# Kernel optimization log

Measured on AMD Instinct MI355X. Metric: run time of the kernel, lower is better.

## Reference

```python
import jax, jax.numpy as jnp
import numpy as np

N = 100000   # nodes
E = 3200000  # edges (avg degree 32)
G = 512      # graphs in batch
F_IN = 10
H = 30


def setup_inputs() -> dict:
    key = jax.random.key(0)
    ks = jax.random.split(key, 14)
    x = jax.random.normal(ks[0], (N, F_IN), dtype=jnp.float32)
    edge_index = jax.random.randint(ks[1], (2, E), 0, N, dtype=jnp.int64)
    batch = jnp.sort(jax.random.randint(ks[2], (N,), 0, G, dtype=jnp.int64))
    edge_weights = jnp.ones((E,), dtype=jnp.float32)
    s = 0.1
    W1 = jax.random.normal(ks[3], (F_IN, H), jnp.float32) * s
    b1 = jnp.zeros((H,), jnp.float32)
    W2 = jax.random.normal(ks[4], (H, H), jnp.float32) * s
    b2 = jnp.zeros((H,), jnp.float32)
    W3 = jax.random.normal(ks[5], (H, H), jnp.float32) * s
    b3 = jnp.zeros((H,), jnp.float32)
    LW1 = jax.random.normal(ks[6], (H, 10), jnp.float32) * s
    Lb1 = jnp.zeros((10,), jnp.float32)
    LW2 = jax.random.normal(ks[7], (10, 2), jnp.float32) * s
    Lb2 = jnp.zeros((2,), jnp.float32)
    return dict(x=x, edge_index=edge_index, batch=batch, edge_weights=edge_weights,
                W1=W1, b1=b1, W2=W2, b2=b2, W3=W3, b3=b3,
                LW1=LW1, Lb1=Lb1, LW2=LW2, Lb2=Lb2)


def reference(x, edge_index, batch, edge_weights, W1, b1, W2, b2, W3, b3, LW1, Lb1, LW2, Lb2):
    n = x.shape[0]
    row, col = edge_index[0], edge_index[1]
    # PyG gcn_norm: add self-loops with weight 1, symmetric normalization
    loop = jnp.arange(n)
    row_f = jnp.concatenate([row, loop])
    col_f = jnp.concatenate([col, loop])
    w_f = jnp.concatenate([edge_weights, jnp.ones((n,), edge_weights.dtype)])
    deg = jax.ops.segment_sum(w_f, col_f, num_segments=n)
    dis = jnp.where(deg > 0, jax.lax.rsqrt(jnp.where(deg > 0, deg, 1.0)), 0.0)
    norm = dis[row_f] * w_f * dis[col_f]  # [E+N]

    def gcn(h, W, b):
        h = h @ W  # [N, out]
        agg = jax.ops.segment_sum(norm[:, None] * h[row_f], col_f, num_segments=n)
        return agg + b

    h = jax.nn.relu(gcn(x, W1, b1))
    h = jax.nn.relu(gcn(h, W2, b2))
    h = jax.nn.relu(gcn(h, W3, b3))  # embedding [N, 30]
    pooled = jax.ops.segment_max(h, batch, num_segments=G)  # [G, 30]
    out = jax.nn.relu(pooled @ LW1 + Lb1) @ LW2 + Lb2  # [G, 2]
    return out
```

## Files before the change

### kernel.cpp

```cpp
#include <hip/hip_runtime.h>
#include <hip/hip_bf16.h>
#include <hip/hip_fp16.h>


#define WG 256
#define CAP 9216
#define T_EDGES 16384

__global__ void k_init(int* bcur, float* pooled, int nb16, int pooledN) {
    int i = blockIdx.x * blockDim.x + threadIdx.x;
    if (i < nb16) bcur[i] = 0;
    if (i < pooledN) pooled[i] = 0.0f;
}

__global__ __launch_bounds__(1024)
void k_bucket(const int* __restrict__ row, const int* __restrict__ col,
              const float* __restrict__ w,
              int* bcur, int2* __restrict__ buck, int E, int NB) {
    __shared__ int hist[512];
    __shared__ int base[512];
    int tid = threadIdx.x;
    for (int i = tid; i < NB; i += 1024) hist[i] = 0;
    __syncthreads();
    int start = blockIdx.x * T_EDGES;
    int end = min(start + T_EDGES, E);
    for (int i = start + tid; i < end; i += 1024)
        atomicAdd(&hist[col[i] >> 8], 1);
    __syncthreads();
    for (int i = tid; i < NB; i += 1024) {
        int h = hist[i];
        base[i] = (h > 0) ? atomicAdd(&bcur[i * 16], h) : 0;
        hist[i] = 0;
    }
    __syncthreads();
    for (int i = start + tid; i < end; i += 1024) {
        int c = col[i];
        int b = c >> 8;
        int off = atomicAdd(&hist[b], 1);
        int pos = base[b] + off;
        if (pos < CAP) {
            int2 pk;
            pk.x = (c & 255) | (row[i] << 8);
            pk.y = __float_as_int(w[i]);
            buck[(size_t)b * CAP + pos] = pk;
        }
    }
}

__global__ __launch_bounds__(1024)
void k_fuse(const int* __restrict__ bcur, const int2* __restrict__ buck,
            float* __restrict__ dis, int* __restrict__ ptr,
            int2* __restrict__ csr, int N, int NB) {
    __shared__ int lc[256];
    __shared__ float lw[256];
    __shared__ int sh[256];
    __shared__ int cur[256];
    __shared__ int sb[512];
    int b = blockIdx.x;
    int tid = threadIdx.x;
    if (tid < 512) sb[tid] = (tid < NB) ? min(bcur[tid * 16], CAP) : 0;
    if (tid < 256) { lc[tid] = 0; lw[tid] = 0.0f; }
    __syncthreads();
    for (int off = 1; off < 512; off <<= 1) {
        int v = (tid < 512 && tid >= off) ? sb[tid - off] : 0;
        __syncthreads();
        if (tid < 512) sb[tid] += v;
        __syncthreads();
    }
    int m = min(bcur[b * 16], CAP);
    int bbase = sb[b] - m;
    if (b == 0 && tid == 0) ptr[N] = sb[511];
    const int2* bp = buck + (size_t)b * CAP;
    for (int i = tid; i < m; i += 1024) {
        int2 pk = bp[i];
        int lcol = pk.x & 255;
        atomicAdd(&lc[lcol], 1);
        atomicAdd(&lw[lcol], __int_as_float(pk.y));
    }
    __syncthreads();
    int lcnt = 0;
    if (tid < 256) { lcnt = lc[tid]; sh[tid] = lcnt; }
    __syncthreads();
    for (int off = 1; off < 256; off <<= 1) {
        int t = (tid >= off && tid < 256) ? sh[tid - off] : 0;
        __syncthreads();
        if (tid < 256) sh[tid] += t;
        __syncthreads();
    }
    int node = (b << 8) + tid;
    if (tid < 256) {
        int base = bbase + sh[tid] - lcnt;
        cur[tid] = base;
        if (node < N) {
            ptr[node] = base;
            float d = 1.0f + lw[tid];
            dis[node] = (d > 0.0f) ? (1.0f / sqrtf(d)) : 0.0f;
        }
    }
    __syncthreads();
    for (int i = tid; i < m; i += 1024) {
        int2 pk = bp[i];
        int lcol = pk.x & 255;
        int pos = atomicAdd(&cur[lcol], 1);
        int2 rec;
        rec.x = (int)(((unsigned)pk.x) >> 8);
        rec.y = pk.y;
        csr[pos] = rec;
    }
}

__global__ void k_stage(const float* __restrict__ x, const float* __restrict__ dis,
                        __half* __restrict__ xp, int n) {
    int gid = blockIdx.x * blockDim.x + threadIdx.x;
    int node = gid >> 4, f = gid & 15;
    if (node < n)
        xp[(size_t)node * 16 + f] = __float2half((f < 10) ? dis[node] * x[(size_t)node * 10 + f] : 0.0f);
}

__global__ __launch_bounds__(256, 4)
void k_agg16(const __half* __restrict__ xp, const float* __restrict__ dis,
             const int* __restrict__ ptr, const int2* __restrict__ csr,
             float* __restrict__ y, int n) {
    int wid = (blockIdx.x * blockDim.x + threadIdx.x) >> 6;
    int lane = threadIdx.x & 63;
    int f = lane & 15;
    int laneq = lane & 48;
    int node = 4 * wid + (lane >> 4);
    bool valid = node < n;
    int s = 0, e = 0;
    if (valid) { s = ptr[node]; e = ptr[node + 1]; }
    int len = e - s;
    int m01 = max(__shfl(len, 0, 64), __shfl(len, 16, 64));
    int m23 = max(__shfl(len, 32, 64), __shfl(len, 48, 64));
    int maxlen = max(m01, m23);
    float a0 = 0.0f, a1 = 0.0f, a2 = 0.0f, a3 = 0.0f;
    for (int off = 0; off < maxlen; off += 16) {
        int idxv = 0; float nrmv = 0.0f;
        if (off + f < len) {
            int2 v = csr[s + off + f];
            idxv = v.x;
            nrmv = __int_as_float(v.y);
        }
        float wt[16], vt[16];
#pragma unroll
        for (int j = 0; j < 16; j++) {
            int r = __shfl(idxv, laneq | j, 64);
            wt[j] = __shfl(nrmv, laneq | j, 64);
            vt[j] = __half2float(xp[(size_t)r * 16 + f]);
        }
#pragma unroll
        for (int j = 0; j < 16; j += 4) {
            a0 = fmaf(wt[j],     vt[j],     a0);
            a1 = fmaf(wt[j + 1], vt[j + 1], a1);
            a2 = fmaf(wt[j + 2], vt[j + 2], a2);
            a3 = fmaf(wt[j + 3], vt[j + 3], a3);
        }
    }
    if (valid) {
        float acc = (a0 + a1) + (a2 + a3);
        float r = dis[node] * (acc + __half2float(xp[(size_t)node * 16 + f]));
        y[(size_t)node * 16 + f] = r;
    }
}

__global__ __launch_bounds__(256)
void k_lin1(const float* __restrict__ y, const float* __restrict__ W1,
            const float* __restrict__ b1, const float* __restrict__ W2,
            const float* __restrict__ dis, __half* __restrict__ out, int n) {
    __shared__ float W1s[10 * 32];
    __shared__ float W2s[30 * 32];
    __shared__ float b1s[32];
    __shared__ float ys[8][16];
    __shared__ float hs[8][32];
    int tid = threadIdx.x;
    for (int i = tid; i < 10 * 32; i += 256) { int k = i >> 5, f = i & 31; W1s[i] = (f < 30) ? W1[k * 30 + f] : 0.0f; }
    for (int i = tid; i < 30 * 32; i += 256) { int k = i >> 5, f = i & 31; W2s[i] = (f < 30) ? W2[k * 30 + f] : 0.0f; }
    if (tid < 32) b1s[tid] = (tid < 30) ? b1[tid] : 0.0f;
    int n8 = tid >> 5, f = tid & 31;
    int node = blockIdx.x * 8 + n8;
    __syncthreads();
    if (node < n && f < 16) ys[n8][f] = y[(size_t)node * 16 + f];
    __syncthreads();
    if (node < n) {
        float h = b1s[f];
#pragma unroll
        for (int k = 0; k < 10; k++) h += ys[n8][k] * W1s[k * 32 + f];
        h = fmaxf(h, 0.0f);
        if (f >= 30) h = 0.0f;
        hs[n8][f] = h;
    }
    __syncthreads();
    if (node < n) {
        float o = 0.0f;
#pragma unroll
        for (int k = 0; k < 30; k++) o += hs[n8][k] * W2s[k * 32 + f];
        out[(size_t)node * 32 + f] = __float2half(o * dis[node]);
    }
}

__global__ void k_matmul30(const float* __restrict__ in,
                           const float* __restrict__ W, const float* __restrict__ dis,
                           __half* __restrict__ out, int n) {
    __shared__ float Ws[30 * 30];
    for (int idx = threadIdx.x; idx < 30 * 30; idx += blockDim.x) Ws[idx] = W[idx];
    __syncthreads();
    int gid = blockIdx.x * blockDim.x + threadIdx.x;
    int node = gid >> 5;
    int f = gid & 31;
    if (node < n) {
        float acc = 0.0f;
        if (f < 30) {
            const float* ip = in + (size_t)node * 32;
#pragma unroll
            for (int k = 0; k < 30; k++) acc += ip[k] * Ws[k * 30 + f];
            acc *= dis[node];
        }
        out[(size_t)node * 32 + f] = __float2half(acc);
    }
}

__global__ __launch_bounds__(256, 4)
void k_agg_store(const __half* __restrict__ hw, const float* __restrict__ dis,
                 const int* __restrict__ ptr, const int2* __restrict__ csr,
                 const float* __restrict__ bias,
                 float* __restrict__ out, int n) {
    int wid = (blockIdx.x * blockDim.x + threadIdx.x) >> 6;
    int lane = threadIdx.x & 63;
    if (wid >= n) return;
    int f = lane & 31;
    int half = lane >> 5;
    int s = ptr[wid];
    int e = ptr[wid + 1];
    float a0 = 0.0f, a1 = 0.0f, a2 = 0.0f, a3 = 0.0f;
    for (int base = s; base < e; base += 32) {
        int idxv = 0; float nrmv = 0.0f;
        int src = base + lane;
        if (lane < 32 && src < e) {
            int2 v = csr[src];
            idxv = v.x;
            nrmv = __int_as_float(v.y);
        }
        float wt[16], vt[16];
#pragma unroll
        for (int j = 0; j < 16; j++) {
            int sl = 2 * j + half;
            int r = __shfl(idxv, sl, 64);
            wt[j] = __shfl(nrmv, sl, 64);
            vt[j] = __half2float(hw[(size_t)r * 32 + f]);
        }
#pragma unroll
        for (int j = 0; j < 16; j += 4) {
            a0 = fmaf(wt[j],     vt[j],     a0);
            a1 = fmaf(wt[j + 1], vt[j + 1], a1);
            a2 = fmaf(wt[j + 2], vt[j + 2], a2);
            a3 = fmaf(wt[j + 3], vt[j + 3], a3);
        }
    }
    float acc = (a0 + a1) + (a2 + a3);
    acc += __shfl_xor(acc, 32, 64);
    float dc = dis[wid];
    float r = dc * (acc + __half2float(hw[(size_t)wid * 32 + f]));
    if (half == 0 && f < 30) {
        r += bias[f];
        out[(size_t)wid * 32 + f] = fmaxf(r, 0.0f);
    }
}

__global__ __launch_bounds__(256, 4)
void k_agg_pool(const __half* __restrict__ hw, const float* __restrict__ dis,
                const int* __restrict__ ptr, const int2* __restrict__ csr,
                const float* __restrict__ bias, const int* __restrict__ batch,
                float* __restrict__ pooled, int n) {
    __shared__ float red[4][32];
    __shared__ int grp[4];
    int wid = (blockIdx.x * blockDim.x + threadIdx.x) >> 6;
    int lane = threadIdx.x & 63;
    int f = lane & 31;
    int half = lane >> 5;
    bool valid = wid < n;
    int s = 0, e = 0;
    if (valid) { s = ptr[wid]; e = ptr[wid + 1]; }
    float a0 = 0.0f, a1 = 0.0f, a2 = 0.0f, a3 = 0.0f;
    for (int base = s; base < e; base += 32) {
        int idxv = 0; float nrmv = 0.0f;
        int src = base + lane;
        if (lane < 32 && src < e) {
            int2 v = csr[src];
            idxv = v.x;
            nrmv = __int_as_float(v.y);
        }
        float wt[16], vt[16];
#pragma unroll
        for (int j = 0; j < 16; j++) {
            int sl = 2 * j + half;
            int r = __shfl(idxv, sl, 64);
            wt[j] = __shfl(nrmv, sl, 64);
            vt[j] = __half2float(hw[(size_t)r * 32 + f]);
        }
#pragma unroll
        for (int j = 0; j < 16; j += 4) {
            a0 = fmaf(wt[j],     vt[j],     a0);
            a1 = fmaf(wt[j + 1], vt[j + 1], a1);
            a2 = fmaf(wt[j + 2], vt[j + 2], a2);
            a3 = fmaf(wt[j + 3], vt[j + 3], a3);
        }
    }
    float acc = (a0 + a1) + (a2 + a3);
    acc += __shfl_xor(acc, 32, 64);
    float rv = 0.0f;
    if (valid && half == 0 && f < 30) {
        float dc = dis[wid];
        float r = dc * (acc + __half2float(hw[(size_t)wid * 32 + f]));
        rv = fmaxf(r + bias[f], 0.0f);
    }
    int w = threadIdx.x >> 6;
    if (half == 0) red[w][f] = rv;
    if (lane == 0) grp[w] = valid ? batch[wid] : -1;
    __syncthreads();
    if (w == 0 && half == 0 && f < 30) {
        int g0 = grp[0], g1 = grp[1], g2 = grp[2], g3 = grp[3];
        if (g0 >= 0 && g0 == g1 && g0 == g2 && g0 == g3) {
            float m = fmaxf(fmaxf(red[0][f], red[1][f]), fmaxf(red[2][f], red[3][f]));
            atomicMax((int*)&pooled[g0 * 32 + f], __float_as_int(m));
        } else {
            if (g0 >= 0) atomicMax((int*)&pooled[g0 * 32 + f], __float_as_int(red[0][f]));
            if (g1 >= 0) atomicMax((int*)&pooled[g1 * 32 + f], __float_as_int(red[1][f]));
            if (g2 >= 0) atomicMax((int*)&pooled[g2 * 32 + f], __float_as_int(red[2][f]));
            if (g3 >= 0) atomicMax((int*)&pooled[g3 * 32 + f], __float_as_int(red[3][f]));
        }
    }
}

__global__ void k_mlp(const float* __restrict__ pooled,
                      const float* __restrict__ LW1, const float* __restrict__ Lb1,
                      const float* __restrict__ LW2, const float* __restrict__ Lb2,
                      float* __restrict__ out, int G) {
    int g = blockIdx.x * blockDim.x + threadIdx.x;
    if (g >= G) return;
    float p[30];
#pragma unroll
    for (int k = 0; k < 30; k++) p[k] = pooled[g * 32 + k];
    float o0 = Lb2[0], o1 = Lb2[1];
#pragma unroll
    for (int j = 0; j < 10; j++) {
        float hj = Lb1[j];
#pragma unroll
        for (int k = 0; k < 30; k++) hj += p[k] * LW1[k * 10 + j];
        hj = fmaxf(hj, 0.0f);
        o0 += hj * LW2[j * 2 + 0];
        o1 += hj * LW2[j * 2 + 1];
    }
    out[g * 2 + 0] = o0;
    out[g * 2 + 1] = o1;
}

extern "C" void kernel_launch(void* const* d_in, const int* in_sizes, int n_in,
                              void* d_out, int out_size, void* d_ws, size_t ws_size,
                              hipStream_t stream) {
    const float* x     = (const float*)d_in[0];
    const int*   ei    = (const int*)d_in[1];
    const int*   batch = (const int*)d_in[2];
    const float* ew    = (const float*)d_in[3];
    const float* W1 = (const float*)d_in[4];  const float* b1  = (const float*)d_in[5];
    const float* W2 = (const float*)d_in[6];  const float* b2  = (const float*)d_in[7];
    const float* W3 = (const float*)d_in[8];  const float* b3  = (const float*)d_in[9];
    const float* LW1 = (const float*)d_in[10]; const float* Lb1 = (const float*)d_in[11];
    const float* LW2 = (const float*)d_in[12]; const float* Lb2 = (const float*)d_in[13];
    float* out = (float*)d_out;

    const int N = in_sizes[2];
    const int E = in_sizes[3];
    const int G = out_size / 2;
    const int* row = ei;
    const int* col = ei + E;

    const int NB = (N + 255) >> 8;

    char* p = (char*)d_ws;
    auto carve = [&](size_t bytes) -> void* {
        void* r = (void*)p;
        p += (bytes + 255) & ~(size_t)255;
        return r;
    };
    int*   ptr       = (int*)carve((size_t)(N + 1) * 4);
    float* dis       = (float*)carve((size_t)N * 4);
    int*   bcur      = (int*)carve((size_t)NB * 16 * 4);
    int2*  csr       = (int2*)carve((size_t)E * 8);
    size_t buckBytes = (size_t)NB * CAP * 8;
    size_t featBytes = (size_t)N * 32 * 4 * 2;
    char*  regionA   = (char*)carve(buckBytes > featBytes ? buckBytes : featBytes);
    int2*  buck      = (int2*)regionA;
    float* bufA      = (float*)regionA;
    __half* xp       = (__half*)regionA;
    float* y16       = (float*)(regionA + (size_t)N * 16 * 2);
    __half* bufB     = (__half*)(regionA + (size_t)N * 32 * 4);
    float* pooled    = (float*)carve((size_t)G * 32 * 4);

    int initN = (NB * 16 > G * 32) ? NB * 16 : G * 32;

    k_init<<<(initN + WG - 1) / WG, WG, 0, stream>>>(bcur, pooled, NB * 16, G * 32);
    k_bucket<<<(E + T_EDGES - 1) / T_EDGES, 1024, 0, stream>>>(row, col, ew, bcur, buck, E, NB);
    k_fuse<<<NB, 1024, 0, stream>>>(bcur, buck, dis, ptr, csr, N, NB);

    int agg_grid   = (int)(((size_t)N * 64 + WG - 1) / WG);
    int agg16_grid = (int)(((size_t)((N + 3) / 4) * 64 + WG - 1) / WG);
    int mm_grid    = (int)(((size_t)N * 32 + WG - 1) / WG);

    k_stage<<<(int)(((size_t)N * 16 + WG - 1) / WG), WG, 0, stream>>>(x, dis, xp, N);
    k_agg16<<<agg16_grid, WG, 0, stream>>>(xp, dis, ptr, csr, y16, N);
    k_lin1<<<(N + 7) / 8, 256, 0, stream>>>(y16, W1, b1, W2, dis, bufB, N);
    k_agg_store<<<agg_grid, WG, 0, stream>>>(bufB, dis, ptr, csr, b2, bufA, N);
    k_matmul30<<<mm_grid, WG, 0, stream>>>(bufA, W3, dis, bufB, N);
    k_agg_pool<<<agg_grid, WG, 0, stream>>>(bufB, dis, ptr, csr, b3, batch, pooled, N);

    k_mlp<<<(G + WG - 1) / WG, WG, 0, stream>>>(pooled, LW1, Lb1, LW2, Lb2, out, G);
}
```

Baseline: 383.4 us.

## Split fp16 feature buffer into two 16-wide planes for the 30-dim aggregations

The 32-wide fp16 node features are now written as two separate planes of 16 features each. Each aggregation block handles one plane, and the block index is interleaved so both halves of a node chunk run close together in time. Each gathered row becomes a 32-byte segment, so the per-plane working set is halved and may fit better in cache. The cost is twice as many CSR index reads and wavefronts per node, plus an extra cross-lane reduction.

```diff
diff --git a/kernel.cpp b/kernel.cpp
--- a/kernel.cpp
+++ b/kernel.cpp
@@ -194,7 +194,9 @@
         float o = 0.0f;
 #pragma unroll
         for (int k = 0; k < 30; k++) o += hs[n8][k] * W2s[k * 32 + f];
-        out[(size_t)node * 32 + f] = __float2half(o * dis[node]);
+        size_t planeElems = (size_t)n * 16;
+        out[(size_t)(f >> 4) * planeElems + (size_t)node * 16 + (f & 15)] =
+            __float2half(o * dis[node]);
     }
 }
 
@@ -215,22 +217,30 @@
             for (int k = 0; k < 30; k++) acc += ip[k] * Ws[k * 30 + f];
             acc *= dis[node];
         }
-        out[(size_t)node * 32 + f] = __float2half(acc);
+        size_t planeElems = (size_t)n * 16;
+        out[(size_t)(f >> 4) * planeElems + (size_t)node * 16 + (f & 15)] =
+            __float2half(acc);
     }
 }
 
 __global__ __launch_bounds__(256, 4)
-void k_agg_store(const __half* __restrict__ hw, const float* __restrict__ dis,
-                 const int* __restrict__ ptr, const int2* __restrict__ csr,
-                 const float* __restrict__ bias,
-                 float* __restrict__ out, int n) {
-    int wid = (blockIdx.x * blockDim.x + threadIdx.x) >> 6;
+void k_agg_store2(const __half* __restrict__ hwp, const float* __restrict__ dis,
+                  const int* __restrict__ ptr, const int2* __restrict__ csr,
+                  const float* __restrict__ bias,
+                  float* __restrict__ out, int n, int C) {
+    int bid = blockIdx.x;
+    int half = bid & 1;
+    int chunk = (bid >> 3) * 4 + ((bid & 7) >> 1);
+    if (chunk >= C) return;
+    int w = threadIdx.x >> 6;
+    int node = chunk * 4 + w;
+    if (node >= n) return;
     int lane = threadIdx.x & 63;
-    if (wid >= n) return;
-    int f = lane & 31;
-    int half = lane >> 5;
-    int s = ptr[wid];
-    int e = ptr[wid + 1];
+    int f16 = lane & 15;
+    int egrp = lane >> 4;
+    const __half* plane = hwp + (size_t)half * ((size_t)n * 16);
+    int s = ptr[node];
+    int e = ptr[node + 1];
     float a0 = 0.0f, a1 = 0.0f, a2 = 0.0f, a3 = 0.0f;
     for (int base = s; base < e; base += 32) {
         int idxv = 0; float nrmv = 0.0f;
@@ -240,16 +250,16 @@
             idxv = v.x;
             nrmv = __int_as_float(v.y);
         }
-        float wt[16], vt[16];
-#pragma unroll
-        for (int j = 0; j < 16; j++) {
-            int sl = 2 * j + half;
+        float wt[8]; float vt[8];
+#pragma unroll
+        for (int j = 0; j < 8; j++) {
+            int sl = 4 * j + egrp;
             int r = __shfl(idxv, sl, 64);
             wt[j] = __shfl(nrmv, sl, 64);
-            vt[j] = __half2float(hw[(size_t)r * 32 + f]);
-        }
-#pragma unroll
-        for (int j = 0; j < 16; j += 4) {
+            vt[j] = __half2float(plane[(size_t)r * 16 + f16]);
+        }
+#pragma unroll
+        for (int j = 0; j < 8; j += 4) {
             a0 = fmaf(wt[j],     vt[j],     a0);
             a1 = fmaf(wt[j + 1], vt[j + 1], a1);
             a2 = fmaf(wt[j + 2], vt[j + 2], a2);
@@ -257,29 +267,35 @@
         }
     }
     float acc = (a0 + a1) + (a2 + a3);
+    acc += __shfl_xor(acc, 16, 64);
     acc += __shfl_xor(acc, 32, 64);
-    float dc = dis[wid];
-    float r = dc * (acc + __half2float(hw[(size_t)wid * 32 + f]));
-    if (half == 0 && f < 30) {
-        r += bias[f];
-        out[(size_t)wid * 32 + f] = fmaxf(r, 0.0f);
+    int f = half * 16 + f16;
+    if (egrp == 0 && f < 30) {
+        float dc = dis[node];
+        float r = dc * (acc + __half2float(plane[(size_t)node * 16 + f16]));
+        out[(size_t)node * 32 + f] = fmaxf(r + bias[f], 0.0f);
     }
 }
 
 __global__ __launch_bounds__(256, 4)
-void k_agg_pool(const __half* __restrict__ hw, const float* __restrict__ dis,
-                const int* __restrict__ ptr, const int2* __restrict__ csr,
-                const float* __restrict__ bias, const int* __restrict__ batch,
-                float* __restrict__ pooled, int n) {
-    __shared__ float red[4][32];
+void k_agg_pool2(const __half* __restrict__ hwp, const float* __restrict__ dis,
+                 const int* __restrict__ ptr, const int2* __restrict__ csr,
+                 const float* __restrict__ bias, const int* __restrict__ batch,
+                 float* __restrict__ pooled, int n, int C) {
+    __shared__ float red[4][16];
     __shared__ int grp[4];
-    int wid = (blockIdx.x * blockDim.x + threadIdx.x) >> 6;
+    int bid = blockIdx.x;
+    int half = bid & 1;
+    int chunk = (bid >> 3) * 4 + ((bid & 7) >> 1);
+    int w = threadIdx.x >> 6;
+    int node = chunk * 4 + w;
+    bool valid = (chunk < C) && (node < n);
     int lane = threadIdx.x & 63;
-    int f = lane & 31;
-    int half = lane >> 5;
-    bool valid = wid < n;
+    int f16 = lane & 15;
+    int egrp = lane >> 4;
+    const __half* plane = hwp + (size_t)half * ((size_t)n * 16);
     int s = 0, e = 0;
-    if (valid) { s = ptr[wid]; e = ptr[wid + 1]; }
+    if (valid) { s = ptr[node]; e = ptr[node + 1]; }
     float a0 = 0.0f, a1 = 0.0f, a2 = 0.0f, a3 = 0.0f;
     for (int base = s; base < e; base += 32) {
         int idxv = 0; float nrmv = 0.0f;
@@ -289,16 +305,16 @@
             idxv = v.x;
             nrmv = __int_as_float(v.y);
         }
-        float wt[16], vt[16];
-#pragma unroll
-        for (int j = 0; j < 16; j++) {
-            int sl = 2 * j + half;
+        float wt[8]; float vt[8];
+#pragma unroll
+        for (int j = 0; j < 8; j++) {
+            int sl = 4 * j + egrp;
             int r = __shfl(idxv, sl, 64);
             wt[j] = __shfl(nrmv, sl, 64);
-            vt[j] = __half2float(hw[(size_t)r * 32 + f]);
-        }
-#pragma unroll
-        for (int j = 0; j < 16; j += 4) {
+            vt[j] = __half2float(plane[(size_t)r * 16 + f16]);
+        }
+#pragma unroll
+        for (int j = 0; j < 8; j += 4) {
             a0 = fmaf(wt[j],     vt[j],     a0);
             a1 = fmaf(wt[j + 1], vt[j + 1], a1);
             a2 = fmaf(wt[j + 2], vt[j + 2], a2);
@@ -306,27 +322,33 @@
         }
     }
     float acc = (a0 + a1) + (a2 + a3);
+    acc += __shfl_xor(acc, 16, 64);
     acc += __shfl_xor(acc, 32, 64);
     float rv = 0.0f;
-    if (valid && half == 0 && f < 30) {
-        float dc = dis[wid];
-        float r = dc * (acc + __half2float(hw[(size_t)wid * 32 + f]));
+    int f = half * 16 + f16;
+    if (valid && lane < 16 && f < 30) {
+        float dc = dis[node];
+        float r = dc * (acc + __half2float(plane[(size_t)node * 16 + f16]));
         rv = fmaxf(r + bias[f], 0.0f);
     }
-    int w = threadIdx.x >> 6;
-    if (half == 0) red[w][f] = rv;
-    if (lane == 0) grp[w] = valid ? batch[wid] : -1;
-    __syncthreads();
-    if (w == 0 && half == 0 && f < 30) {
-        int g0 = grp[0], g1 = grp[1], g2 = grp[2], g3 = grp[3];
-        if (g0 >= 0 && g0 == g1 && g0 == g2 && g0 == g3) {
-            float m = fmaxf(fmaxf(red[0][f], red[1][f]), fmaxf(red[2][f], red[3][f]));
-            atomicMax((int*)&pooled[g0 * 32 + f], __float_as_int(m));
-        } else {
-            if (g0 >= 0) atomicMax((int*)&pooled[g0 * 32 + f], __float_as_int(red[0][f]));
-            if (g1 >= 0) atomicMax((int*)&pooled[g1 * 32 + f], __float_as_int(red[1][f]));
-            if (g2 >= 0) atomicMax((int*)&pooled[g2 * 32 + f], __float_as_int(red[2][f]));
-            if (g3 >= 0) atomicMax((int*)&pooled[g3 * 32 + f], __float_as_int(red[3][f]));
+    if (lane < 16) red[w][lane] = rv;
+    if (lane == 0) grp[w] = valid ? batch[node] : -1;
+    __syncthreads();
+    if (w == 0 && threadIdx.x < 16) {
+        int ff = half * 16 + (int)threadIdx.x;
+        if (ff < 30) {
+            int g0 = grp[0], g1 = grp[1], g2 = grp[2], g3 = grp[3];
+            float r0 = red[0][threadIdx.x], r1 = red[1][threadIdx.x];
+            float r2 = red[2][threadIdx.x], r3 = red[3][threadIdx.x];
+            if (g0 >= 0 && g0 == g1 && g0 == g2 && g0 == g3) {
+                float m = fmaxf(fmaxf(r0, r1), fmaxf(r2, r3));
+                atomicMax((int*)&pooled[g0 * 32 + ff], __float_as_int(m));
+            } else {
+                if (g0 >= 0) atomicMax((int*)&pooled[g0 * 32 + ff], __float_as_int(r0));
+                if (g1 >= 0) atomicMax((int*)&pooled[g1 * 32 + ff], __float_as_int(r1));
+                if (g2 >= 0) atomicMax((int*)&pooled[g2 * 32 + ff], __float_as_int(r2));
+                if (g3 >= 0) atomicMax((int*)&pooled[g3 * 32 + ff], __float_as_int(r3));
+            }
         }
     }
 }
@@ -402,16 +424,17 @@
     k_bucket<<<(E + T_EDGES - 1) / T_EDGES, 1024, 0, stream>>>(row, col, ew, bcur, buck, E, NB);
     k_fuse<<<NB, 1024, 0, stream>>>(bcur, buck, dis, ptr, csr, N, NB);
 
-    int agg_grid   = (int)(((size_t)N * 64 + WG - 1) / WG);
     int agg16_grid = (int)(((size_t)((N + 3) / 4) * 64 + WG - 1) / WG);
     int mm_grid    = (int)(((size_t)N * 32 + WG - 1) / WG);
+    const int C    = (N + 3) / 4;
+    int agg2_grid  = ((C + 3) / 4) * 8;
 
     k_stage<<<(int)(((size_t)N * 16 + WG - 1) / WG), WG, 0, stream>>>(x, dis, xp, N);
     k_agg16<<<agg16_grid, WG, 0, stream>>>(xp, dis, ptr, csr, y16, N);
     k_lin1<<<(N + 7) / 8, 256, 0, stream>>>(y16, W1, b1, W2, dis, bufB, N);
-    k_agg_store<<<agg_grid, WG, 0, stream>>>(bufB, dis, ptr, csr, b2, bufA, N);
+    k_agg_store2<<<agg2_grid, WG, 0, stream>>>(bufB, dis, ptr, csr, b2, bufA, N, C);
     k_matmul30<<<mm_grid, WG, 0, stream>>>(bufA, W3, dis, bufB, N);
-    k_agg_pool<<<agg_grid, WG, 0, stream>>>(bufB, dis, ptr, csr, b3, batch, pooled, N);
+    k_agg_pool2<<<agg2_grid, WG, 0, stream>>>(bufB, dis, ptr, csr, b3, batch, pooled, N, C);
 
     k_mlp<<<(G + WG - 1) / WG, WG, 0, stream>>>(pooled, LW1, Lb1, LW2, Lb2, out, G);
 }
```

Result: slower. 419.6 us (+9.5%).
